# Kernel optimization log

Measured on AMD Instinct MI355X. Metric: run time of the kernel, lower is better.

The kernel has to match this reference:

```python
import jax, jax.numpy as jnp
import numpy as np

D = 4
KERNEL = (3, 3, 3, 3)
CIN = 8
COUT = 16
SPATIAL = (24, 24, 24, 24)
B = 8


def setup_inputs() -> dict:
    key = jax.random.key(0)
    k1, k2, k3 = jax.random.split(key, 3)
    x = jax.random.normal(k1, (B, CIN) + SPATIAL, dtype=jnp.float32)
    kmul = int(np.prod(KERNEL))  # 81
    # torch layout: zeros(O, kmul, 1).repeat(1,1,Cin).reshape(O, kmul*Cin)
    # -> flat dim is kernel-major, channel-minor
    weight = jax.random.normal(k2, (COUT, kmul * CIN), dtype=jnp.float32) * 0.05
    bias = jax.random.normal(k3, (COUT,), dtype=jnp.float32) * 0.05
    return {"x": x, "weight": weight, "bias": bias}


def reference(x, weight, bias):
    # Unflatten weight to (O, k1, k2, k3, k4, Cin) matching the unfold's
    # (kernel..., channel) flatten order, then run a direct 4-D 'same' conv
    # (cross-correlation, identical math to the unfold+matmul original).
    w = weight.reshape((COUT,) + KERNEL + (CIN,))
    dn = jax.lax.ConvDimensionNumbers(
        lhs_spec=(0, 1, 2, 3, 4, 5),   # N, C, s1..s4
        rhs_spec=(0, 5, 1, 2, 3, 4),   # O, I, k1..k4  (I lives at axis 5 of w)
        out_spec=(0, 1, 2, 3, 4, 5),   # N, O, s1..s4
    )
    out = jax.lax.conv_general_dilated(
        x, w,
        window_strides=(1,) * D,
        padding=[(1, 1)] * D,
        dimension_numbers=dn,
    )
    return out + bias.reshape((1, COUT) + (1,) * D)
```

## Files before the change

kernel.cpp:

```cpp
#include <hip/hip_runtime.h>
#include <hip/hip_bf16.h>


#define SDIM  24
#define SP    (SDIM * SDIM * SDIM * SDIM)
#define PD    26
#define SPPAD (PD * PD * PD * PD)
#define CIN   8
#define COUT  16
#define BATCH 8
#define KW    648
#define NCHUNK 21
#define NB    4
#define PTILES (SP / 16)
#define NBLOCKS ((BATCH / NB) * PTILES / 4)

#define ZERO_OFF 0
#define WPK_OFF  256
#define XT_OFF   32768
#define XT_BYTES  ((size_t)BATCH * SP * CIN * 2)
#define XTP_BYTES ((size_t)BATCH * SPPAD * CIN * 2)
#define WS_NEEDED_OLD (XT_OFF + XT_BYTES)
#define WS_NEEDED_PAD (XT_OFF + XTP_BYTES)

#define HALO_PER_B   125200
#define HROW_SLOTS   97552
#define HALO_TOTAL   (BATCH * HALO_PER_B)
#define HBLOCKS      3913
#define TBLOCKS      (BATCH * SP / 4 / 256)
#define WBLOCKS      6
#define PREP_BLOCKS  (HBLOCKS + TBLOCKS + WBLOCKS)

typedef __attribute__((ext_vector_type(8))) short short8;
typedef __attribute__((ext_vector_type(4))) float f32x4;

static __device__ __forceinline__ unsigned short f2bf(float f) {
    unsigned u = __builtin_bit_cast(unsigned, f);
    u = (u + 0x7fffu + ((u >> 16) & 1u)) >> 16;
    return (unsigned short)u;
}

__global__ __launch_bounds__(256) void prep_fused(
    const float* __restrict__ x, const float* __restrict__ w,
    unsigned char* __restrict__ ws)
{
    const int bid = blockIdx.x;
    const int tid = threadIdx.x;

    if (bid < HBLOCKS) {
        int t = bid * 256 + tid;
        if (t >= HALO_TOTAL) return;
        int b = t / HALO_PER_B;
        int h = t - b * HALO_PER_B;
        int q1, q2, q3, q4;
        if (h < HROW_SLOTS) {
            int rid = h / 26;
            q4 = h - rid * 26;
            if (rid < 1352) {
                q1 = (rid < 676) ? 0 : 25;
                int rr = rid % 676;
                q2 = rr / 26; q3 = rr - (rr / 26) * 26;
            } else if (rid < 2600) {
                int r2 = rid - 1352;
                q1 = 1 + r2 / 52;
                int rr = r2 - (r2 / 52) * 52;
                q2 = (rr < 26) ? 0 : 25;
                q3 = rr % 26;
            } else {
                int r3 = rid - 2600;
                q1 = 1 + r3 / 48;
                int rr = r3 - (r3 / 48) * 48;
                q2 = 1 + rr / 2;
                q3 = (rr & 1) ? 25 : 0;
            }
        } else {
            int e = h - HROW_SLOTS;
            int rid = e >> 1;
            q4 = (e & 1) ? 25 : 0;
            q1 = 1 + rid / 576;
            int rr = rid - (rid / 576) * 576;
            q2 = 1 + rr / 24;
            q3 = 1 + rr - (rr / 24) * 24;
        }
        size_t slot = (size_t)b * SPPAD + (((q1 * PD + q2) * PD + q3) * PD + q4);
        short8 z = {0, 0, 0, 0, 0, 0, 0, 0};
        ((short8*)(ws + XT_OFF))[slot] = z;
        return;
    }

    if (bid < HBLOCKS + TBLOCKS) {
        int idx = (bid - HBLOCKS) * 256 + tid;
        int b  = idx / (SP / 4);
        int pq = idx - b * (SP / 4);
        int p  = pq * 4;
        const float* xb = x + (size_t)b * CIN * SP + p;

        float4 v[CIN];
        #pragma unroll
        for (int c = 0; c < CIN; ++c)
            v[c] = *(const float4*)(xb + (size_t)c * SP);

        union { __hip_bfloat162 h2[4]; short8 s8; } u[4];
        #pragma unroll
        for (int j = 0; j < 4; ++j) {
            #pragma unroll
            for (int i = 0; i < 4; ++i) {
                float a0 = (&v[2 * i].x)[j];
                float a1 = (&v[2 * i + 1].x)[j];
                u[j].h2[i] = __float22bfloat162_rn(make_float2(a0, a1));
            }
        }

        int r = p;
        const int p4 = r % SDIM; r /= SDIM;
        const int p3 = r % SDIM; r /= SDIM;
        const int p2 = r % SDIM;
        const int p1 = r / SDIM;
        int qp = (((p1 + 1) * PD + (p2 + 1)) * PD + (p3 + 1)) * PD + (p4 + 1);

        short8* dst = (short8*)(ws + XT_OFF) + (size_t)b * SPPAD + qp;
        #pragma unroll
        for (int j = 0; j < 4; ++j) dst[j] = u[j].s8;
        return;
    }

    int t = (bid - HBLOCKS - TBLOCKS) * 256 + tid;
    if (t >= NCHUNK * 64) return;
    int chunk = t >> 6;
    int lane  = t & 63;
    int m     = lane & 15;
    int quad  = lane >> 4;
    short8 pk;
    #pragma unroll
    for (int j = 0; j < 8; ++j) {
        int k = chunk * 32 + quad * 8 + j;
        float f = (k < KW) ? w[m * KW + k] : 0.0f;
        pk[j] = (short)f2bf(f);
    }
    ((short8*)(ws + WPK_OFF))[chunk * 64 + lane] = pk;
}

__global__ __launch_bounds__(256) void conv4d_mfma_pad(
    const unsigned char* __restrict__ ws,
    const float* __restrict__ bias,
    float* __restrict__ out)
{
    __shared__ int    s_delta[96];
    __shared__ short8 s_w[NCHUNK * 64];

    const int tid  = threadIdx.x;
    const int lane = tid & 63;
    const int wave = tid >> 6;
    const int col  = lane & 15;
    const int quad = lane >> 4;

    const short8* wpk = (const short8*)(ws + WPK_OFF);
    for (int t = tid; t < NCHUNK * 64; t += 256) s_w[t] = wpk[t];
    if (tid < 84) {
        int k1 = tid / 27, rem = tid - k1 * 27;
        int k2 = rem / 9;  rem -= k2 * 9;
        int k3 = rem / 3;
        int k4 = rem - k3 * 3;
        s_delta[tid] = (k1 * (PD * PD * PD) + k2 * (PD * PD) + k3 * PD + k4) * 16;
    }
    __syncthreads();

    int W = blockIdx.x * 4 + wave;
    W = __builtin_amdgcn_readfirstlane(W);
    const int pt = W % PTILES;
    const int g  = W / PTILES;

    const int p = pt * 16 + col;
    int r = p;
    const int p4 = r % SDIM; r /= SDIM;
    const int p3 = r % SDIM; r /= SDIM;
    const int p2 = r % SDIM;
    const int p1 = r / SDIM;
    const int pidx16 = (((p1 * PD + p2) * PD + p3) * PD + p4) * 16;

    const unsigned char* xbase[NB];
    #pragma unroll
    for (int t = 0; t < NB; ++t)
        xbase[t] = ws + XT_OFF + (size_t)(g * NB + t) * SPPAD * 16;

    int voffs[NCHUNK];
    #pragma unroll
    for (int c = 0; c < NCHUNK; ++c)
        voffs[c] = pidx16 + s_delta[c * 4 + quad];

    f32x4 acc[NB];
    #pragma unroll
    for (int t = 0; t < NB; ++t) acc[t] = (f32x4){0.f, 0.f, 0.f, 0.f};

    short8 bf[2][NB];
    #pragma unroll
    for (int t = 0; t < NB; ++t)
        bf[0][t] = *(const short8*)(xbase[t] + voffs[0]);

    #pragma unroll
    for (int c = 0; c < NCHUNK; ++c) {
        const int cur = c & 1;
        const int nxt = cur ^ 1;
        if (c + 1 < NCHUNK) {
            #pragma unroll
            for (int t = 0; t < NB; ++t)
                bf[nxt][t] = *(const short8*)(xbase[t] + voffs[c + 1]);
        }
        short8 afrag = s_w[c * 64 + lane];
        #pragma unroll
        for (int t = 0; t < NB; ++t)
            acc[t] = __builtin_amdgcn_mfma_f32_16x16x32_bf16(afrag, bf[cur][t], acc[t], 0, 0, 0);
    }

    f32x4 b4 = *(const f32x4*)(bias + quad * 4);
    #pragma unroll
    for (int t = 0; t < NB; ++t) {
        float* obase = out + ((size_t)(g * NB + t) * COUT + quad * 4) * SP + p;
        #pragma unroll
        for (int reg = 0; reg < 4; ++reg)
            obase[(size_t)reg * SP] = acc[t][reg] + b4[reg];
    }
}


__global__ __launch_bounds__(256) void pack_weights(
    const float* __restrict__ w, unsigned char* __restrict__ ws)
{
    int t = blockIdx.x * 256 + threadIdx.x;
    if (t == 1344) {
        short8 z = {0,0,0,0,0,0,0,0};
        *(short8*)(ws + ZERO_OFF) = z;
    }
    if (t >= NCHUNK * 64) return;
    int chunk = t >> 6;
    int lane  = t & 63;
    int m     = lane & 15;
    int quad  = lane >> 4;
    short8 pk;
    #pragma unroll
    for (int j = 0; j < 8; ++j) {
        int k = chunk * 32 + quad * 8 + j;
        float f = (k < KW) ? w[m * KW + k] : 0.0f;
        pk[j] = (short)f2bf(f);
    }
    ((short8*)(ws + WPK_OFF))[chunk * 64 + lane] = pk;
}

__global__ __launch_bounds__(256) void transpose_x(
    const float* __restrict__ x, unsigned char* __restrict__ ws)
{
    int idx = blockIdx.x * 256 + threadIdx.x;
    int b  = idx / (SP / 2);
    int pp = idx - b * (SP / 2);
    int p  = pp * 2;
    const float* xb = x + (size_t)b * CIN * SP + p;

    float2 v[CIN];
    #pragma unroll
    for (int c = 0; c < CIN; ++c)
        v[c] = *(const float2*)(xb + (size_t)c * SP);

    union { __hip_bfloat162 h2[4]; short8 s8; } u0, u1;
    #pragma unroll
    for (int i = 0; i < 4; ++i) {
        float2 a = make_float2(v[2 * i].x, v[2 * i + 1].x);
        float2 bq = make_float2(v[2 * i].y, v[2 * i + 1].y);
        u0.h2[i] = __float22bfloat162_rn(a);
        u1.h2[i] = __float22bfloat162_rn(bq);
    }
    short8* dst = (short8*)(ws + XT_OFF) + ((size_t)b * SP + p);
    dst[0] = u0.s8;
    dst[1] = u1.s8;
}

__global__ __launch_bounds__(256) void conv4d_mfma(
    const unsigned char* __restrict__ ws,
    const float* __restrict__ bias,
    float* __restrict__ out)
{
    const int lane = threadIdx.x & 63;
    const int wave = threadIdx.x >> 6;
    const int col  = lane & 15;
    const int quad = lane >> 4;

    int W = blockIdx.x * 4 + wave;
    W = __builtin_amdgcn_readfirstlane(W);
    const int pt = W % PTILES;
    const int g  = W / PTILES;

    const int p = pt * 16 + col;
    int r = p;
    const int p4 = r % SDIM; r /= SDIM;
    const int p3 = r % SDIM; r /= SDIM;
    const int p2 = r % SDIM;
    const int p1 = r / SDIM;

    const short8* wpk  = (const short8*)(ws + WPK_OFF);
    const short8* xT   = (const short8*)(ws + XT_OFF);
    const short8* zslt = (const short8*)(ws + ZERO_OFF);

    const short8* xb[NB];
    #pragma unroll
    for (int t = 0; t < NB; ++t)
        xb[t] = xT + (size_t)(g * NB + t) * SP;

    f32x4 acc[NB];
    #pragma unroll
    for (int t = 0; t < NB; ++t) acc[t] = (f32x4){0.f, 0.f, 0.f, 0.f};

    #pragma unroll
    for (int c = 0; c < NCHUNK; ++c) {
        short8 afrag = wpk[c * 64 + lane];

        int tap = c * 4 + quad;
        int k1 = tap / 27; int rem = tap - k1 * 27;
        int k2 = rem / 9;  rem -= k2 * 9;
        int k3 = rem / 3;
        int k4 = rem - k3 * 3;
        int q1 = p1 + k1 - 1, q2 = p2 + k2 - 1, q3 = p3 + k3 - 1, q4 = p4 + k4 - 1;
        bool valid = ((unsigned)q1 < (unsigned)SDIM) & ((unsigned)q2 < (unsigned)SDIM) &
                     ((unsigned)q3 < (unsigned)SDIM) & ((unsigned)q4 < (unsigned)SDIM);
        int q = ((q1 * SDIM + q2) * SDIM + q3) * SDIM + q4;

        short8 bf[NB];
        #pragma unroll
        for (int t = 0; t < NB; ++t) {
            const short8* src = valid ? (xb[t] + q) : zslt;
            bf[t] = *src;
        }
        #pragma unroll
        for (int t = 0; t < NB; ++t)
            acc[t] = __builtin_amdgcn_mfma_f32_16x16x32_bf16(afrag, bf[t], acc[t], 0, 0, 0);
    }

    f32x4 b4 = *(const f32x4*)(bias + quad * 4);
    #pragma unroll
    for (int t = 0; t < NB; ++t) {
        float* obase = out + ((size_t)(g * NB + t) * COUT + quad * 4) * SP + p;
        #pragma unroll
        for (int reg = 0; reg < 4; ++reg)
            obase[(size_t)reg * SP] = acc[t][reg] + b4[reg];
    }
}

__global__ __launch_bounds__(256) void conv4d_direct(
    const float* __restrict__ x, const float* __restrict__ w,
    const float* __restrict__ bias, float* __restrict__ out)
{
    int t = blockIdx.x * blockDim.x + threadIdx.x;
    int b = t / SP;
    int p = t - b * SP;
    int p4 = p % SDIM; int tmp = p / SDIM;
    int p3 = tmp % SDIM; tmp /= SDIM;
    int p2 = tmp % SDIM; int p1 = tmp / SDIM;
    float acc[COUT];
    #pragma unroll
    for (int o = 0; o < COUT; ++o) acc[o] = bias[o];
    const float* xb = x + (size_t)b * CIN * SP;
    for (int k1 = 0; k1 < 3; ++k1) {
        unsigned q1 = (unsigned)(p1 + k1 - 1); if (q1 >= SDIM) continue;
        for (int k2 = 0; k2 < 3; ++k2) {
            unsigned q2 = (unsigned)(p2 + k2 - 1); if (q2 >= SDIM) continue;
            for (int k3 = 0; k3 < 3; ++k3) {
                unsigned q3 = (unsigned)(p3 + k3 - 1); if (q3 >= SDIM) continue;
                int base123 = (((int)q1 * SDIM + (int)q2) * SDIM + (int)q3) * SDIM;
                int kf = ((k1 * 3 + k2) * 3 + k3) * 3;
                for (int k4 = 0; k4 < 3; ++k4) {
                    unsigned q4 = (unsigned)(p4 + k4 - 1); if (q4 >= SDIM) continue;
                    int q = base123 + (int)q4;
                    float xv[CIN];
                    #pragma unroll
                    for (int c = 0; c < CIN; ++c) xv[c] = xb[c * SP + q];
                    const float* wp = w + (kf + k4) * CIN;
                    #pragma unroll
                    for (int o = 0; o < COUT; ++o)
                        #pragma unroll
                        for (int c = 0; c < CIN; ++c)
                            acc[o] = fmaf(xv[c], wp[o * KW + c], acc[o]);
                }
            }
        }
    }
    float* ob = out + (size_t)b * COUT * SP + p;
    #pragma unroll
    for (int o = 0; o < COUT; ++o) ob[o * SP] = acc[o];
}

extern "C" void kernel_launch(void* const* d_in, const int* in_sizes, int n_in,
                              void* d_out, int out_size, void* d_ws, size_t ws_size,
                              hipStream_t stream)
{
    const float* x    = (const float*)d_in[0];
    const float* w    = (const float*)d_in[1];
    const float* bias = (const float*)d_in[2];
    float* out        = (float*)d_out;
    unsigned char* ws = (unsigned char*)d_ws;

    if (ws_size >= WS_NEEDED_PAD) {
        hipLaunchKernelGGL(prep_fused, dim3(PREP_BLOCKS), dim3(256), 0, stream,
                           x, w, ws);
        hipLaunchKernelGGL(conv4d_mfma_pad, dim3(NBLOCKS), dim3(256), 0, stream,
                           (const unsigned char*)ws, bias, out);
        return;
    }

    if (ws_size >= WS_NEEDED_OLD) {
        hipLaunchKernelGGL(pack_weights, dim3(6), dim3(256), 0, stream, w, ws);
        const int pair_total = BATCH * SP / 2;
        hipLaunchKernelGGL(transpose_x, dim3(pair_total / 256), dim3(256), 0, stream, x, ws);
        hipLaunchKernelGGL(conv4d_mfma, dim3(NBLOCKS), dim3(256), 0, stream,
                           (const unsigned char*)ws, bias, out);
        return;
    }

    const int total = BATCH * SP;
    hipLaunchKernelGGL(conv4d_direct, dim3(total / 256), dim3(256), 0, stream,
                       x, w, bias, out);
}
```

Before: 356.7 us.

## Stage padded input halo tile in LDS and compute conv from shared memory

Replaces the per-wave direct global gathers of the padded bf16 input with a block-level tiling. Each block covers one (p1,p2) row and an 8x8 patch of (p3,p4) for 4 batches, and loads a 3x3x10x10 halo per batch into LDS. The MFMA loop then reads B fragments from LDS, so the 81-tap overlap is served on chip instead of re-fetched from L2/global memory. In exchange it uses about 58KB of LDS per block (launch bounds request 2 blocks), adds a barrier-gated load phase with no overlap against compute, and gives each block only a 64-position output tile.

New measurement: 453.1 us. 27.0% more time.

```diff
diff --git a/kernel.cpp b/kernel.cpp
--- a/kernel.cpp
+++ b/kernel.cpp
@@ -13,7 +13,9 @@
 #define NCHUNK 21
 #define NB    4
 #define PTILES (SP / 16)
-#define NBLOCKS ((BATCH / NB) * PTILES / 4)
+#define NBLOCKS_OLD ((BATCH / NB) * PTILES / 4)
+
+#define NBLK  (2 * 24 * 24 * 3 * 3)
 
 #define ZERO_OFF 0
 #define WPK_OFF  256
@@ -140,82 +142,86 @@
     ((short8*)(ws + WPK_OFF))[chunk * 64 + lane] = pk;
 }
 
-__global__ __launch_bounds__(256) void conv4d_mfma_pad(
+__global__ __launch_bounds__(256, 2) void conv4d_lds(
     const unsigned char* __restrict__ ws,
     const float* __restrict__ bias,
     float* __restrict__ out)
 {
-    __shared__ int    s_delta[96];
+    __shared__ short8 s_x[4 * 900];
     __shared__ short8 s_w[NCHUNK * 64];
+    __shared__ int    s_dly[96];
 
     const int tid  = threadIdx.x;
     const int lane = tid & 63;
     const int wave = tid >> 6;
     const int col  = lane & 15;
     const int quad = lane >> 4;
+    const int c3   = col >> 2;
+    const int c4   = col & 3;
+    const int wt3  = wave >> 1;
+    const int wt4  = wave & 1;
+
+    int bid = __builtin_amdgcn_readfirstlane((int)blockIdx.x);
+    const int g  = bid / 5184;  int r = bid - g * 5184;
+    const int p1 = r / 216;     r -= p1 * 216;
+    const int p2 = r / 9;       int s = r - p2 * 9;
+    const int S3 = (s / 3) * 8;
+    const int S4 = (s % 3) * 8;
 
     const short8* wpk = (const short8*)(ws + WPK_OFF);
     for (int t = tid; t < NCHUNK * 64; t += 256) s_w[t] = wpk[t];
     if (tid < 84) {
-        int k1 = tid / 27, rem = tid - k1 * 27;
-        int k2 = rem / 9;  rem -= k2 * 9;
-        int k3 = rem / 3;
-        int k4 = rem - k3 * 3;
-        s_delta[tid] = (k1 * (PD * PD * PD) + k2 * (PD * PD) + k3 * PD + k4) * 16;
+        if (tid >= 81) {
+            s_dly[tid] = 0;
+        } else {
+            int k1 = tid / 27, rem = tid - k1 * 27;
+            int k2 = rem / 9;  rem -= k2 * 9;
+            int k3 = rem / 3;
+            int k4 = rem - k3 * 3;
+            s_dly[tid] = ((k1 * 3 + k2) * 10 + k3) * 10 + k4;
+        }
+    }
+
+    const short8* xT = (const short8*)(ws + XT_OFF);
+    for (int t = tid; t < 3600; t += 256) {
+        int b  = t / 900;
+        int rr = t - b * 900;
+        int d1 = rr / 300;  rr -= d1 * 300;
+        int d2 = rr / 100;  rr -= d2 * 100;
+        int r3 = rr / 10;
+        int r4 = rr - r3 * 10;
+        size_t gq = (((size_t)(p1 + d1) * PD + (p2 + d2)) * PD + (S3 + r3)) * PD + (S4 + r4);
+        s_x[t] = xT[(size_t)(g * NB + b) * SPPAD + gq];
     }
     __syncthreads();
 
-    int W = blockIdx.x * 4 + wave;
-    W = __builtin_amdgcn_readfirstlane(W);
-    const int pt = W % PTILES;
-    const int g  = W / PTILES;
-
-    const int p = pt * 16 + col;
-    int r = p;
-    const int p4 = r % SDIM; r /= SDIM;
-    const int p3 = r % SDIM; r /= SDIM;
-    const int p2 = r % SDIM;
-    const int p1 = r / SDIM;
-    const int pidx16 = (((p1 * PD + p2) * PD + p3) * PD + p4) * 16;
-
-    const unsigned char* xbase[NB];
-    #pragma unroll
-    for (int t = 0; t < NB; ++t)
-        xbase[t] = ws + XT_OFF + (size_t)(g * NB + t) * SPPAD * 16;
-
-    int voffs[NCHUNK];
-    #pragma unroll
-    for (int c = 0; c < NCHUNK; ++c)
-        voffs[c] = pidx16 + s_delta[c * 4 + quad];
+    const int lane_off = (wt3 * 4 + c3) * 10 + (wt4 * 4 + c4);
 
     f32x4 acc[NB];
     #pragma unroll
     for (int t = 0; t < NB; ++t) acc[t] = (f32x4){0.f, 0.f, 0.f, 0.f};
 
-    short8 bf[2][NB];
-    #pragma unroll
-    for (int t = 0; t < NB; ++t)
-        bf[0][t] = *(const short8*)(xbase[t] + voffs[0]);
-
     #pragma unroll
     for (int c = 0; c < NCHUNK; ++c) {
-        const int cur = c & 1;
-        const int nxt = cur ^ 1;
-        if (c + 1 < NCHUNK) {
-            #pragma unroll
-            for (int t = 0; t < NB; ++t)
-                bf[nxt][t] = *(const short8*)(xbase[t] + voffs[c + 1]);
-        }
         short8 afrag = s_w[c * 64 + lane];
+        int bidx = s_dly[c * 4 + quad] + lane_off;
+
+        short8 bf[NB];
         #pragma unroll
         for (int t = 0; t < NB; ++t)
-            acc[t] = __builtin_amdgcn_mfma_f32_16x16x32_bf16(afrag, bf[cur][t], acc[t], 0, 0, 0);
-    }
-
+            bf[t] = s_x[t * 900 + bidx];
+        #pragma unroll
+        for (int t = 0; t < NB; ++t)
+            acc[t] = __builtin_amdgcn_mfma_f32_16x16x32_bf16(afrag, bf[t], acc[t], 0, 0, 0);
+    }
+
+    const int p3 = S3 + wt3 * 4 + c3;
+    const int p4 = S4 + wt4 * 4 + c4;
+    const size_t pos = (((size_t)p1 * SDIM + p2) * SDIM + p3) * SDIM + p4;
     f32x4 b4 = *(const f32x4*)(bias + quad * 4);
     #pragma unroll
     for (int t = 0; t < NB; ++t) {
-        float* obase = out + ((size_t)(g * NB + t) * COUT + quad * 4) * SP + p;
+        float* obase = out + ((size_t)(g * NB + t) * COUT + quad * 4) * SP + pos;
         #pragma unroll
         for (int reg = 0; reg < 4; ++reg)
             obase[(size_t)reg * SP] = acc[t][reg] + b4[reg];
@@ -399,7 +405,7 @@
     if (ws_size >= WS_NEEDED_PAD) {
         hipLaunchKernelGGL(prep_fused, dim3(PREP_BLOCKS), dim3(256), 0, stream,
                            x, w, ws);
-        hipLaunchKernelGGL(conv4d_mfma_pad, dim3(NBLOCKS), dim3(256), 0, stream,
+        hipLaunchKernelGGL(conv4d_lds, dim3(NBLK), dim3(256), 0, stream,
                            (const unsigned char*)ws, bias, out);
         return;
     }
@@ -408,7 +414,7 @@
         hipLaunchKernelGGL(pack_weights, dim3(6), dim3(256), 0, stream, w, ws);
         const int pair_total = BATCH * SP / 2;
         hipLaunchKernelGGL(transpose_x, dim3(pair_total / 256), dim3(256), 0, stream, x, ws);
-        hipLaunchKernelGGL(conv4d_mfma, dim3(NBLOCKS), dim3(256), 0, stream,
+        hipLaunchKernelGGL(conv4d_mfma, dim3(NBLOCKS_OLD), dim3(256), 0, stream,
                            (const unsigned char*)ws, bias, out);
         return;
     }
```
